# Kernel tuning notes

Measured on AMD Instinct MI355X. Metric: run time of the kernel, lower is better.

The kernel has to match this reference:

```python
import jax, jax.numpy as jnp
import numpy as np

B = 524288      # batch
F = 32          # nr_features
C = 10          # nr_classes
H = 64          # hidden_size
D = 2           # tree_depth
NN = 2 ** D - 1 # internal nodes
NL = 2 ** D     # leaf nodes
EPS = 1e-5

# Static tree routing tables, reproducing the original Python int() (truncate-toward-zero) math exactly.
NODE_IDX = np.array([[int((2 ** (d - 1) * (2 ** D + l) - 2 ** D) / 2 ** D) for d in range(D)] for l in range(NL)])  # [NL, D]
PSIGN = np.array([[int(l / 2 ** (D - d)) % 2 for d in range(D)] for l in range(NL)])  # [NL, D]


def _linear_params(key, out_f, in_f):
    k1, k2 = jax.random.split(key)
    bound = 1.0 / np.sqrt(in_f)
    w = jax.random.uniform(k1, (out_f, in_f), minval=-bound, maxval=bound, dtype=jnp.float32)
    b = jax.random.uniform(k2, (out_f,), minval=-bound, maxval=bound, dtype=jnp.float32)
    return w, b


def setup_inputs() -> dict:
    key = jax.random.key(0)
    ks = jax.random.split(key, 6)
    x = jax.random.normal(ks[0], (B, F), dtype=jnp.float32)
    w_in, b_in = _linear_params(ks[1], H, F)
    bn_g = jnp.ones((H,), dtype=jnp.float32)   # BatchNorm1d weight init to 1
    bn_b = jnp.zeros((H,), dtype=jnp.float32)  # BatchNorm1d bias init to 0
    w_fi, b_fi = _linear_params(ks[2], NN * F, H)
    w_fs, b_fs = _linear_params(ks[3], NN * F, H)
    w_lc, b_lc = _linear_params(ks[4], NL * C, H)
    return {"x": x, "w_in": w_in, "b_in": b_in, "bn_g": bn_g, "bn_b": bn_b,
            "w_fi": w_fi, "b_fi": b_fi, "w_fs": w_fs, "b_fs": b_fs,
            "w_lc": w_lc, "b_lc": b_lc}


def reference(x, w_in, b_in, bn_g, bn_b, w_fi, b_fi, w_fs, b_fs, w_lc, b_lc):
    inp = x  # raw features used inside the tree gating
    # input layer + BatchNorm1d (training-mode batch stats, biased var) + exact GELU
    h = x @ w_in.T + b_in                                   # [B, H]
    mu = jnp.mean(h, axis=0)
    var = jnp.var(h, axis=0)
    h = (h - mu) / jnp.sqrt(var + EPS) * bn_g + bn_b
    h = jax.nn.gelu(h, approximate=False)

    fi = (h @ w_fi.T + b_fi).reshape(B, NN, F)              # feature importances per node
    fs = (h @ w_fs.T + b_fs).reshape(B, NN, F)              # feature splits per node
    lc = (h @ w_lc.T + b_lc).reshape(B, NL, C)              # leaf class logits

    smx = jax.nn.softmax(fi, axis=-1)                        # [B, NN, F]
    # node_sd = sigmoid(sum(smx*input) - sum(smx*fs))
    sd = jax.nn.sigmoid(jnp.einsum('bnf,bnf->bn', smx, inp[:, None, :] - fs))  # [B, NN]

    # gate per (leaf, depth): sd if p==0 else 1-sd, at the statically-computed node index
    g = sd[:, NODE_IDX]                                      # [B, NL, D]
    g = jnp.where(PSIGN[None, :, :] == 0, g, 1.0 - g)
    coeff = jnp.prod(g, axis=-1)                             # [B, NL]

    out = jnp.einsum('blc,bl->bc', lc, coeff)                # [B, C]
    return out
```

## Files before the change

### kernel.cpp

```cpp
#include <hip/hip_runtime.h>

typedef __attribute__((ext_vector_type(8))) __bf16 bf16x8;
typedef __attribute__((ext_vector_type(4))) float f32x4;
typedef __attribute__((ext_vector_type(8))) unsigned short u16x8;
typedef unsigned short u16;
typedef unsigned int u32;

#define NB 524288
#define EPSI 1e-5f
#define NSHADOW 16
#define K_LOG2E 1.4426950408889634f


__device__ __forceinline__ float bf2f(u16 h) {
    union { u32 u; float f; } cv; cv.u = ((u32)h) << 16; return cv.f;
}
__device__ __forceinline__ u16 f2bf(float f) {
    __bf16 b = (__bf16)f; return __builtin_bit_cast(u16, b);
}
__device__ __forceinline__ float ldany(const void* p, long i, int isf) {
    return isf ? ((const float*)p)[i] : bf2f(((const u16*)p)[i]);
}

#if __has_builtin(__builtin_amdgcn_exp2f)
#define EXP2F(x) __builtin_amdgcn_exp2f(x)
#else
#define EXP2F(x) exp2f(x)
#endif

#define GK1 2.3022082f
#define GK2 0.10294324f
__device__ __forceinline__ float fast_gelu(float v) {
    float t2 = v * fmaf(GK2, v * v, GK1);
    float en = EXP2F(-t2);
    return v * __builtin_amdgcn_rcpf(1.0f + en);
}

__device__ __forceinline__ bf16x8 loadfrag(const __bf16* p) {
    return *reinterpret_cast<const bf16x8*>(p);
}
__device__ __forceinline__ bf16x8 loadfrag(const float* p) {
    f32x4 a = *reinterpret_cast<const f32x4*>(p);
    f32x4 b = *reinterpret_cast<const f32x4*>(p + 4);
    bf16x8 r;
#pragma unroll
    for (int i = 0; i < 4; ++i) { r[i] = (__bf16)a[i]; r[4 + i] = (__bf16)b[i]; }
    return r;
}

__device__ __forceinline__ void load2f(const float* p, float& a, float& b) {
    const float2 v = *reinterpret_cast<const float2*>(p);
    a = v.x; b = v.y;
}
__device__ __forceinline__ void load2f(const __bf16* p, float& a, float& b) {
    u32 w = *reinterpret_cast<const u32*>(p);
    a = bf2f((u16)(w & 0xffffu)); b = bf2f((u16)(w >> 16));
}

__device__ __forceinline__ int detect_isf(const void* x) {
    const int lane = threadIdx.x & 63;
    u32 w0 = ((const u32*)x)[lane];
    u32 w1 = ((const u32*)x)[64 + lane];
    int hit = ((((w0 >> 7) & 0xFFu) >= 0xC0u) || (((w1 >> 7) & 0xFFu) >= 0xC0u)) ? 1 : 0;
    return __ballot(hit) != 0ull;
}

template<int CTRL>
__device__ __forceinline__ float dpp_rot_add(float v) {
    int s = __builtin_amdgcn_update_dpp(0, __builtin_bit_cast(int, v), CTRL, 0xF, 0xF, false);
    return v + __builtin_bit_cast(float, s);
}
__device__ __forceinline__ float row_reduce_add(float v) {
    v = dpp_rot_add<0x121>(v);
    v = dpp_rot_add<0x122>(v);
    v = dpp_rot_add<0x124>(v);
    v = dpp_rot_add<0x128>(v);
    return v;
}

template<typename T>
__device__ __forceinline__ void stats_body(const T* __restrict__ x,
                                           const T* __restrict__ w_in,
                                           float* __restrict__ ws,
                                           float* __restrict__ red) {
    const int lane = threadIdx.x & 63;
    const int wave = threadIdx.x >> 6;
    const int c = lane & 15;
    const int q = lane >> 4;

    bf16x8 b1[4];
#pragma unroll
    for (int nt = 0; nt < 4; ++nt)
        b1[nt] = loadfrag(w_in + (nt * 16 + c) * 32 + q * 8);

    float accs[4][4], accq[4][4];
#pragma unroll
    for (int nt = 0; nt < 4; ++nt)
#pragma unroll
        for (int r = 0; r < 4; ++r) { accs[nt][r] = 0.f; accq[nt][r] = 0.f; }

    const int wid = blockIdx.x * 4 + wave;
#pragma unroll
    for (int t = 0; t < 4; ++t) {
        const long row0 = ((long)wid * 4 + t) * 16;
        bf16x8 a1 = loadfrag(x + (row0 + c) * 32 + q * 8);
#pragma unroll
        for (int nt = 0; nt < 4; ++nt) {
            f32x4 z = {0.f, 0.f, 0.f, 0.f};
            f32x4 acc = __builtin_amdgcn_mfma_f32_16x16x32_bf16(a1, b1[nt], z, 0, 0, 0);
#pragma unroll
            for (int r = 0; r < 4; ++r) {
                float v = acc[r];
                accs[nt][r] += v;
                accq[nt][r] += v * v;
            }
        }
    }
    for (int i = threadIdx.x; i < 128; i += 256) red[i] = 0.f;
    __syncthreads();
#pragma unroll
    for (int nt = 0; nt < 4; ++nt) {
        float s  = accs[nt][0] + accs[nt][1] + accs[nt][2] + accs[nt][3];
        float sq = accq[nt][0] + accq[nt][1] + accq[nt][2] + accq[nt][3];
        s  += __shfl_xor(s, 16);  s  += __shfl_xor(s, 32);
        sq += __shfl_xor(sq, 16); sq += __shfl_xor(sq, 32);
        if (q == 0) {
            atomicAdd(&red[nt * 16 + c], s);
            atomicAdd(&red[64 + nt * 16 + c], sq);
        }
    }
    __syncthreads();
    float* shard = ws + (blockIdx.x & (NSHADOW - 1)) * 128;
    for (int i = threadIdx.x; i < 128; i += 256) atomicAdd(&shard[i], red[i]);
}

__global__ __launch_bounds__(256) void stats_kernel(
    const void* x, const void* w_in, float* __restrict__ ws)
{
    const int isf = detect_isf(x);
    __shared__ float red[128];
    if (isf) stats_body<float>((const float*)x, (const float*)w_in, ws, red);
    else     stats_body<__bf16>((const __bf16*)x, (const __bf16*)w_in, ws, red);
}

__global__ __launch_bounds__(256) void finalize_kernel(
    const void* x, const void* w_in, const void* bn_g, const void* bn_b,
    const void* w_fi, const void* b_fi, const void* w_fs, const void* b_fs,
    const void* w_lc, const void* b_lc, float* __restrict__ ws)
{
    const int isf = detect_isf(x);
    const int tid = threadIdx.x;
    __shared__ float sbuf[128], scl[64], sft[64];

    if (tid < 128) {
        float s = 0.f;
#pragma unroll
        for (int k = 0; k < NSHADOW; ++k) s += ws[k * 128 + tid];
        sbuf[tid] = s;
    }
    __syncthreads();
    if (tid < 64) {
        float mu  = sbuf[tid] * (1.0f / NB);
        float var = fmaxf(sbuf[64 + tid] * (1.0f / NB) - mu * mu, 0.0f);
        float s   = ldany(bn_g, tid, isf) * rsqrtf(var + EPSI);
        scl[tid] = s;
        sft[tid] = ldany(bn_b, tid, isf) - mu * s;
    }
    __syncthreads();
    u16* blob = (u16*)((char*)ws + 16384);
    {
        const int nt = tid >> 6, l = tid & 63, cc = l & 15, qq = l >> 4;
        const int row = 32 * (nt >> 1) + 8 * (cc >> 2) + 4 * (nt & 1) + (cc & 3);
        const float s = scl[row];
        u16x8 v8;
#pragma unroll
        for (int j = 0; j < 8; ++j)
            v8[j] = f2bf(ldany(w_in, row * 32 + qq * 8 + j, isf) * s);
        *reinterpret_cast<u16x8*>(blob + tid * 8) = v8;
    }
    for (int k = tid; k < 768; k += 256) {
        const int f = k >> 6, l = k & 63, cc = l & 15, qq = l >> 4;
        const int nt = f >> 1, kt = f & 1;
        const int hb = kt * 32 + qq * 8;
        u16x8 v8;
        if (nt < 2) {
            const int ft = 2 * cc + nt;
#pragma unroll
            for (int j = 0; j < 8; ++j)
                v8[j] = f2bf(ldany(w_fi, ft * 64 + hb + j, isf) * K_LOG2E);
        } else if (nt < 4) {
            const int ft = 2 * cc + (nt - 2);
#pragma unroll
            for (int j = 0; j < 8; ++j)
                v8[j] = f2bf(ldany(w_fs, ft * 64 + hb + j, isf) * K_LOG2E);
        } else {
            const int r0 = ((nt == 4) ? 0 : 20) + cc;
#pragma unroll
            for (int j = 0; j < 8; ++j)
                v8[j] = (cc < 10) ? f2bf(ldany(w_lc, (long)r0 * 64 + hb + j, isf)
                                       + ldany(w_lc, (long)(r0 + 10) * 64 + hb + j, isf))
                                  : (u16)0;
        }
        *reinterpret_cast<u16x8*>(blob + 2048 + k * 8) = v8;
    }
    float* shsp  = (float*)((char*)ws + 16384 + 16384);
    float* biasp = shsp + 64;
    if (tid < 64) {
        const int qq = tid >> 4, nt = (tid >> 2) & 3, r = tid & 3;
        const int ft = 32 * (nt >> 1) + 8 * qq + 4 * (nt & 1) + r;
        shsp[tid] = sft[ft];
    }
    for (int idx = tid; idx < 384; idx += 256) {
        const int p = idx >> 2, nt = p >> 4, cc = p & 15;
        float v = 0.f;
        if      (nt == 0) v = ldany(b_fi, 2 * cc,     isf) * K_LOG2E;
        else if (nt == 1) v = ldany(b_fi, 2 * cc + 1, isf) * K_LOG2E;
        else if (nt == 2) v = ldany(b_fs, 2 * cc,     isf) * K_LOG2E;
        else if (nt == 3) v = ldany(b_fs, 2 * cc + 1, isf) * K_LOG2E;
        else if (nt == 4) v = (cc < 10) ? ldany(b_lc, cc,      isf) + ldany(b_lc, 10 + cc, isf) : 0.f;
        else              v = (cc < 10) ? ldany(b_lc, 20 + cc, isf) + ldany(b_lc, 30 + cc, isf) : 0.f;
        biasp[idx] = v;
    }
    if (tid < 64) biasp[384 + tid] = 0.f;
}

template<typename T>
__device__ __forceinline__ void main_body(
    const T* __restrict__ x, const float* __restrict__ ws, T* __restrict__ out,
    char* __restrict__ lds)
{
    const int tid = threadIdx.x;
    const int lane = tid & 63;
    const int wave = tid >> 6;
    const int c = lane & 15;
    const int q = lane >> 4;

    const long gw = (long)blockIdx.x * 4 + wave;
    const long rowb = gw * 32;

    bf16x8 a1p0 = loadfrag(x + (rowb + c) * 32 + q * 8);
    bf16x8 a1p1 = loadfrag(x + (rowb + 16 + c) * 32 + q * 8);

    {
        const f32x4* gsrc = (const f32x4*)((const char*)ws + 16384);
        f32x4* ldst = (f32x4*)lds;
        for (int i = tid; i < 1152; i += 256) ldst[i] = gsrc[i];
    }
    __syncthreads();

    bf16x8 w1r[4];
#pragma unroll
    for (int nt = 0; nt < 4; ++nt)
        w1r[nt] = *reinterpret_cast<const bf16x8*>((const u16*)lds + (nt * 64 + lane) * 8);

#pragma unroll
    for (int t = 0; t < 2; ++t) {
        u32 tweak = 0;
        asm volatile("" : "+v"(tweak));
        const u16*   w2b = (const u16*)(lds + 4096) + tweak;
        const float* shb = (const float*)(lds + 16384) + tweak;
        const float* bb  = (const float*)(lds + 16640) + tweak;

        const long row0 = rowb + (long)t * 16;
        const bf16x8 a1 = (t == 0) ? a1p0 : a1p1;

        float xv0[4], xv1[4];
#pragma unroll
        for (int r = 0; r < 4; ++r)
            load2f(x + (row0 + q * 4 + r) * 32 + 2 * c, xv0[r], xv1[r]);

        f32x4 h4[4];
#pragma unroll
        for (int nt = 0; nt < 4; ++nt) {
            f32x4 sh = *reinterpret_cast<const f32x4*>(shb + q * 16 + nt * 4);
            h4[nt] = __builtin_amdgcn_mfma_f32_16x16x32_bf16(w1r[nt], a1, sh, 0, 0, 0);
        }

        bf16x8 a2_0, a2_1;
#pragma unroll
        for (int nt = 0; nt < 2; ++nt) {
#pragma unroll
            for (int r = 0; r < 4; ++r) {
                a2_0[nt * 4 + r] = (__bf16)fast_gelu(h4[nt][r]);
                a2_1[nt * 4 + r] = (__bf16)fast_gelu(h4[2 + nt][r]);
            }
        }

        f32x4 acc[6];
#pragma unroll
        for (int nt = 0; nt < 6; ++nt) {
            bf16x8 f0 = *reinterpret_cast<const bf16x8*>(w2b + ((nt * 2 + 0) * 64 + lane) * 8);
            bf16x8 f1 = *reinterpret_cast<const bf16x8*>(w2b + ((nt * 2 + 1) * 64 + lane) * 8);
            f32x4 bz = *reinterpret_cast<const f32x4*>(bb + (nt * 16 + c) * 4);
            acc[nt] = __builtin_amdgcn_mfma_f32_16x16x32_bf16(a2_0, f0, bz, 0, 0, 0);
            acc[nt] = __builtin_amdgcn_mfma_f32_16x16x32_bf16(a2_1, f1, acc[nt], 0, 0, 0);
        }

#pragma unroll
        for (int r = 0; r < 4; ++r) {
            float e0 = EXP2F(acc[0][r]);
            float e1 = EXP2F(acc[1][r]);
            float t0 = fmaf(K_LOG2E, xv0[r], -acc[2][r]);
            float t1 = fmaf(K_LOG2E, xv1[r], -acc[3][r]);
            float es = row_reduce_add(e0 + e1);
            float dp = row_reduce_add(fmaf(e1, t1, e0 * t0));
            float d2 = dp * __builtin_amdgcn_rcpf(es);
            float sd = __builtin_amdgcn_rcpf(1.0f + EXP2F(-d2));
            float o  = sd * fmaf(sd, acc[4][r] - acc[5][r], acc[5][r]);
            if (c < 10) out[(row0 + q * 4 + r) * 10 + c] = (T)o;
        }
    }
}

__global__ __launch_bounds__(256, 4) void main_kernel(
    const void* x, const float* __restrict__ ws, void* outv)
{
    __shared__ __attribute__((aligned(16))) char lds[18432];
    if (detect_isf(x))
        main_body<float>((const float*)x, ws, (float*)outv, lds);
    else
        main_body<__bf16>((const __bf16*)x, ws, (__bf16*)outv, lds);
}

extern "C" void kernel_launch(void* const* d_in, const int* in_sizes, int n_in,
                              void* d_out, int out_size, void* d_ws, size_t ws_size,
                              hipStream_t stream) {
    float* ws = (float*)d_ws;
    hipMemsetAsync(d_ws, 0, 8192, stream);
    stats_kernel<<<2048, 256, 0, stream>>>(d_in[0], d_in[1], ws);
    finalize_kernel<<<1, 256, 0, stream>>>(d_in[0], d_in[1], d_in[3], d_in[4],
                                           d_in[5], d_in[6], d_in[7], d_in[8],
                                           d_in[9], d_in[10], ws);
    main_kernel<<<4096, 256, 0, stream>>>(d_in[0], ws, d_out);
}
```

Baseline: 160.1 us.

## Eliminate finalize kernel by folding weight prep into stats and BN finalize into main

Removes the single-block finalize launch. The second-layer weight blob and biases are now written by the first few blocks of the stats kernel, since they do not depend on batch statistics. Each main-kernel block reduces the sharded sums itself, computes the BN scale and shift, and builds the scaled first-layer weights in LDS. This cuts one launch and its serial gap, at the cost of redundant per-block finalize work and an extra block synchronisation in every one of the 4096 main blocks.

```diff
diff --git a/kernel.cpp b/kernel.cpp
--- a/kernel.cpp
+++ b/kernel.cpp
@@ -46,6 +46,22 @@
 #pragma unroll
     for (int i = 0; i < 4; ++i) { r[i] = (__bf16)a[i]; r[4 + i] = (__bf16)b[i]; }
     return r;
+}
+
+template<typename T>
+__device__ __forceinline__ void load8f(const T* p, float* o);
+template<>
+__device__ __forceinline__ void load8f<__bf16>(const __bf16* p, float* o) {
+    bf16x8 r = *reinterpret_cast<const bf16x8*>(p);
+#pragma unroll
+    for (int i = 0; i < 8; ++i) o[i] = (float)r[i];
+}
+template<>
+__device__ __forceinline__ void load8f<float>(const float* p, float* o) {
+    f32x4 a = *reinterpret_cast<const f32x4*>(p);
+    f32x4 b = *reinterpret_cast<const f32x4*>(p + 4);
+#pragma unroll
+    for (int i = 0; i < 4; ++i) { o[i] = a[i]; o[4 + i] = b[i]; }
 }
 
 __device__ __forceinline__ void load2f(const float* p, float& a, float& b) {
@@ -135,50 +151,15 @@
 }
 
 __global__ __launch_bounds__(256) void stats_kernel(
-    const void* x, const void* w_in, float* __restrict__ ws)
-{
-    const int isf = detect_isf(x);
-    __shared__ float red[128];
-    if (isf) stats_body<float>((const float*)x, (const float*)w_in, ws, red);
-    else     stats_body<__bf16>((const __bf16*)x, (const __bf16*)w_in, ws, red);
-}
-
-__global__ __launch_bounds__(256) void finalize_kernel(
-    const void* x, const void* w_in, const void* bn_g, const void* bn_b,
+    const void* x, const void* w_in,
     const void* w_fi, const void* b_fi, const void* w_fs, const void* b_fs,
     const void* w_lc, const void* b_lc, float* __restrict__ ws)
 {
     const int isf = detect_isf(x);
     const int tid = threadIdx.x;
-    __shared__ float sbuf[128], scl[64], sft[64];
-
-    if (tid < 128) {
-        float s = 0.f;
-#pragma unroll
-        for (int k = 0; k < NSHADOW; ++k) s += ws[k * 128 + tid];
-        sbuf[tid] = s;
-    }
-    __syncthreads();
-    if (tid < 64) {
-        float mu  = sbuf[tid] * (1.0f / NB);
-        float var = fmaxf(sbuf[64 + tid] * (1.0f / NB) - mu * mu, 0.0f);
-        float s   = ldany(bn_g, tid, isf) * rsqrtf(var + EPSI);
-        scl[tid] = s;
-        sft[tid] = ldany(bn_b, tid, isf) - mu * s;
-    }
-    __syncthreads();
-    u16* blob = (u16*)((char*)ws + 16384);
-    {
-        const int nt = tid >> 6, l = tid & 63, cc = l & 15, qq = l >> 4;
-        const int row = 32 * (nt >> 1) + 8 * (cc >> 2) + 4 * (nt & 1) + (cc & 3);
-        const float s = scl[row];
-        u16x8 v8;
-#pragma unroll
-        for (int j = 0; j < 8; ++j)
-            v8[j] = f2bf(ldany(w_in, row * 32 + qq * 8 + j, isf) * s);
-        *reinterpret_cast<u16x8*>(blob + tid * 8) = v8;
-    }
-    for (int k = tid; k < 768; k += 256) {
+
+    if (blockIdx.x < 3) {
+        const int k = blockIdx.x * 256 + tid;
         const int f = k >> 6, l = k & 63, cc = l & 15, qq = l >> 4;
         const int nt = f >> 1, kt = f & 1;
         const int hb = kt * 32 + qq * 8;
@@ -201,33 +182,34 @@
                                        + ldany(w_lc, (long)(r0 + 10) * 64 + hb + j, isf))
                                   : (u16)0;
         }
-        *reinterpret_cast<u16x8*>(blob + 2048 + k * 8) = v8;
-    }
-    float* shsp  = (float*)((char*)ws + 16384 + 16384);
-    float* biasp = shsp + 64;
-    if (tid < 64) {
-        const int qq = tid >> 4, nt = (tid >> 2) & 3, r = tid & 3;
-        const int ft = 32 * (nt >> 1) + 8 * qq + 4 * (nt & 1) + r;
-        shsp[tid] = sft[ft];
-    }
-    for (int idx = tid; idx < 384; idx += 256) {
-        const int p = idx >> 2, nt = p >> 4, cc = p & 15;
-        float v = 0.f;
-        if      (nt == 0) v = ldany(b_fi, 2 * cc,     isf) * K_LOG2E;
-        else if (nt == 1) v = ldany(b_fi, 2 * cc + 1, isf) * K_LOG2E;
-        else if (nt == 2) v = ldany(b_fs, 2 * cc,     isf) * K_LOG2E;
-        else if (nt == 3) v = ldany(b_fs, 2 * cc + 1, isf) * K_LOG2E;
-        else if (nt == 4) v = (cc < 10) ? ldany(b_lc, cc,      isf) + ldany(b_lc, 10 + cc, isf) : 0.f;
-        else              v = (cc < 10) ? ldany(b_lc, 20 + cc, isf) + ldany(b_lc, 30 + cc, isf) : 0.f;
-        biasp[idx] = v;
-    }
-    if (tid < 64) biasp[384 + tid] = 0.f;
+        *reinterpret_cast<u16x8*>((u16*)((char*)ws + 16384) + k * 8) = v8;
+    } else if (blockIdx.x == 3) {
+        float* biasp = (float*)((char*)ws + 28672);
+        for (int idx = tid; idx < 384; idx += 256) {
+            const int p = idx >> 2, nt = p >> 4, cc = p & 15;
+            float v = 0.f;
+            if      (nt == 0) v = ldany(b_fi, 2 * cc,     isf) * K_LOG2E;
+            else if (nt == 1) v = ldany(b_fi, 2 * cc + 1, isf) * K_LOG2E;
+            else if (nt == 2) v = ldany(b_fs, 2 * cc,     isf) * K_LOG2E;
+            else if (nt == 3) v = ldany(b_fs, 2 * cc + 1, isf) * K_LOG2E;
+            else if (nt == 4) v = (cc < 10) ? ldany(b_lc, cc,      isf) + ldany(b_lc, 10 + cc, isf) : 0.f;
+            else              v = (cc < 10) ? ldany(b_lc, 20 + cc, isf) + ldany(b_lc, 30 + cc, isf) : 0.f;
+            biasp[idx] = v;
+        }
+    }
+
+    __shared__ float red[128];
+    if (isf) stats_body<float>((const float*)x, (const float*)w_in, ws, red);
+    else     stats_body<__bf16>((const __bf16*)x, (const __bf16*)w_in, ws, red);
 }
 
 template<typename T>
 __device__ __forceinline__ void main_body(
-    const T* __restrict__ x, const float* __restrict__ ws, T* __restrict__ out,
-    char* __restrict__ lds)
+    const T* __restrict__ x, const T* __restrict__ w_in,
+    const T* __restrict__ bn_g, const T* __restrict__ bn_b,
+    const float* __restrict__ ws, T* __restrict__ out,
+    char* __restrict__ lds, float* __restrict__ sums,
+    float* __restrict__ scl, float* __restrict__ shs)
 {
     const int tid = threadIdx.x;
     const int lane = tid & 63;
@@ -243,8 +225,38 @@
 
     {
         const f32x4* gsrc = (const f32x4*)((const char*)ws + 16384);
-        f32x4* ldst = (f32x4*)lds;
-        for (int i = tid; i < 1152; i += 256) ldst[i] = gsrc[i];
+        f32x4* ldst = (f32x4*)(lds + 4096);
+        for (int i = tid; i < 864; i += 256) ldst[i] = gsrc[i];
+    }
+    if (tid < 128) {
+        float s = 0.f;
+#pragma unroll
+        for (int k = 0; k < NSHADOW; ++k) s += ws[k * 128 + tid];
+        sums[tid] = s;
+    }
+    __syncthreads();
+
+    if (tid < 64) {
+        const int qq = tid >> 4, nt = (tid >> 2) & 3, r = tid & 3;
+        const int ft = 32 * (nt >> 1) + 8 * qq + 4 * (nt & 1) + r;
+        float mu  = sums[ft] * (1.0f / NB);
+        float var = fmaxf(sums[64 + ft] * (1.0f / NB) - mu * mu, 0.0f);
+        float s   = (float)bn_g[ft] * rsqrtf(var + EPSI);
+        scl[ft] = s;
+        shs[tid] = (float)bn_b[ft] - mu * s;
+    }
+    __syncthreads();
+
+    {
+        const int nt = tid >> 6, l = tid & 63, cc = l & 15, qq = l >> 4;
+        const int row = 32 * (nt >> 1) + 8 * (cc >> 2) + 4 * (nt & 1) + (cc & 3);
+        const float s = scl[row];
+        float w8[8];
+        load8f(w_in + row * 32 + qq * 8, w8);
+        u16x8 v8;
+#pragma unroll
+        for (int j = 0; j < 8; ++j) v8[j] = f2bf(w8[j] * s);
+        *reinterpret_cast<u16x8*>(lds + tid * 16) = v8;
     }
     __syncthreads();
 
@@ -258,8 +270,8 @@
         u32 tweak = 0;
         asm volatile("" : "+v"(tweak));
         const u16*   w2b = (const u16*)(lds + 4096) + tweak;
-        const float* shb = (const float*)(lds + 16384) + tweak;
-        const float* bb  = (const float*)(lds + 16640) + tweak;
+        const float* bb  = (const float*)(lds + 16384) + tweak;
+        const float* shb = shs + tweak;
 
         const long row0 = rowb + (long)t * 16;
         const bf16x8 a1 = (t == 0) ? a1p0 : a1p1;
@@ -313,13 +325,17 @@
 }
 
 __global__ __launch_bounds__(256, 4) void main_kernel(
-    const void* x, const float* __restrict__ ws, void* outv)
+    const void* x, const void* w_in, const void* bn_g, const void* bn_b,
+    const float* __restrict__ ws, void* outv)
 {
-    __shared__ __attribute__((aligned(16))) char lds[18432];
+    __shared__ __attribute__((aligned(16))) char lds[17920];
+    __shared__ float sums[128], scl[64], shs[64];
     if (detect_isf(x))
-        main_body<float>((const float*)x, ws, (float*)outv, lds);
+        main_body<float>((const float*)x, (const float*)w_in, (const float*)bn_g,
+                         (const float*)bn_b, ws, (float*)outv, lds, sums, scl, shs);
     else
-        main_body<__bf16>((const __bf16*)x, ws, (__bf16*)outv, lds);
+        main_body<__bf16>((const __bf16*)x, (const __bf16*)w_in, (const __bf16*)bn_g,
+                          (const __bf16*)bn_b, ws, (__bf16*)outv, lds, sums, scl, shs);
 }
 
 extern "C" void kernel_launch(void* const* d_in, const int* in_sizes, int n_in,
@@ -327,9 +343,9 @@
                               hipStream_t stream) {
     float* ws = (float*)d_ws;
     hipMemsetAsync(d_ws, 0, 8192, stream);
-    stats_kernel<<<2048, 256, 0, stream>>>(d_in[0], d_in[1], ws);
-    finalize_kernel<<<1, 256, 0, stream>>>(d_in[0], d_in[1], d_in[3], d_in[4],
+    stats_kernel<<<2048, 256, 0, stream>>>(d_in[0], d_in[1],
                                            d_in[5], d_in[6], d_in[7], d_in[8],
                                            d_in[9], d_in[10], ws);
-    main_kernel<<<4096, 256, 0, stream>>>(d_in[0], ws, d_out);
-}
+    main_kernel<<<4096, 256, 0, stream>>>(d_in[0], d_in[1], d_in[3], d_in[4],
+                                          ws, d_out);
+}
```

New measurement: 157.2 us. About the same (-1.8%).
